# Kernel tuning notes

Hardware: AMD Instinct MI355X
Metric: run time of the kernel (lower is better)

## Reference

```python
import jax, jax.numpy as jnp
import numpy as np

B, S, H, R = 32, 1024, 1024, 53
EPS = 1e-12
ATT_EPS = 1e10


def setup_inputs() -> dict:
    key = jax.random.key(0)
    ks = jax.random.split(key, 20)
    sc = 0.02
    n = lambda k, shape: jax.random.normal(k, shape, jnp.float32) * sc
    return {
        "relation": jax.random.randint(ks[0], (B, 1), 0, R),
        "last_hidden_size": jax.random.normal(ks[1], (B, S, H), jnp.float32),
        "sub_head": jax.random.randint(ks[2], (B, 1), 0, S),
        "sub_tail": jax.random.randint(ks[3], (B, 1), 0, S),
        "attention_mask": jax.random.randint(ks[4], (B, S), 0, 2).astype(jnp.int32),
        # learned params
        "rel_emb": n(ks[5], (R, H)),
        "Wrf": n(ks[6], (H, H)), "brf": jnp.zeros((H,), jnp.float32),
        "cln_w": jnp.ones((H,), jnp.float32), "cln_b": jnp.zeros((H,), jnp.float32),
        "Wwd": n(ks[7], (H, 2 * H)), "Wbd": n(ks[8], (H, 2 * H)),
        "Wq": n(ks[9], (H, H)), "bq": jnp.zeros((H,), jnp.float32),
        "Wk": n(ks[10], (H, H)), "bk": jnp.zeros((H,), jnp.float32),
        "Wv": n(ks[11], (H, H)), "bv": jnp.zeros((H,), jnp.float32),
        "Wo": n(ks[12], (1, H)), "bo": jnp.zeros((1,), jnp.float32),
    }


def reference(relation, last_hidden_size, sub_head, sub_tail, attention_mask,
              rel_emb, Wrf, brf, cln_w, cln_b, Wwd, Wbd,
              Wq, bq, Wk, bk, Wv, bv, Wo, bo):
    x = last_hidden_size  # [B,S,H]; dropout is identity at inference
    # relation feature: embedding -> linear -> ReLU6
    rel = jnp.clip(jnp.einsum('boh,gh->bog', rel_emb[relation], Wrf) + brf, 0.0, 6.0)  # [B,1,H]
    # gather subject head/tail token features
    bidx = jnp.arange(x.shape[0])[:, None]
    sub = (x[bidx, sub_head] + x[bidx, sub_tail]) * 0.5  # [B,1,H]
    cond = jnp.concatenate([rel, sub], axis=-1)  # [B,1,2H]
    # conditional layer norm: per-example weight/bias generated from cond
    w = jnp.einsum('boc,gc->bog', cond, Wwd) + cln_w  # [B,1,H]
    b = jnp.einsum('boc,gc->bog', cond, Wbd) + cln_b  # [B,1,H]
    mean = jnp.mean(x, axis=-1, keepdims=True)
    c = x - mean
    var = jnp.mean(c * c, axis=-1, keepdims=True)
    normed = c / jnp.sqrt(var + EPS) * w + b  # [B,S,H]
    # ReLU-activated QKV attention with additive mask bias and residual
    q = jax.nn.relu(jnp.einsum('bsh,gh->bsg', normed, Wq) + bq)
    k = jax.nn.relu(jnp.einsum('bsh,gh->bsg', normed, Wk) + bk)
    v = jax.nn.relu(jnp.einsum('bsh,gh->bsg', normed, Wv) + bv)
    e = jnp.einsum('bsh,bth->bst', q, k)  # [B,S,S]
    m = attention_mask.astype(e.dtype)[:, None, :]  # [B,1,S]
    e = e - ATT_EPS * (1.0 - m)
    a = jax.nn.softmax(e, axis=-1)
    hidden = jnp.einsum('bst,bth->bsh', a, v) + normed  # [B,S,H]
    pred_obj_head = (jnp.einsum('bsh,gh->bsg', hidden, Wo) + bo)[..., 0]  # [B,S]
    return (pred_obj_head, hidden)
```

## Files before the change

### kernel.cpp

```cpp
#include <hip/hip_runtime.h>
#include <hip/hip_bf16.h>
#include <hip/hip_fp16.h>

#define NB 32
#define NS 1024
#define NH 1024

typedef short s16x4 __attribute__((ext_vector_type(4)));
typedef short s16x8 __attribute__((ext_vector_type(8)));
typedef float f32x4 __attribute__((ext_vector_type(4)));

typedef __attribute__((address_space(3))) void lds_void;
typedef const __attribute__((address_space(1))) void gmem_void;

__device__ __forceinline__ short f2bf(float f) {
  __hip_bfloat16 h = __float2bfloat16(f);
  return *reinterpret_cast<short*>(&h);
}
__device__ __forceinline__ float bf2f(short s) {
  union { unsigned u; float f; } cv;
  cv.u = ((unsigned)(unsigned short)s) << 16;
  return cv.f;
}
__device__ __forceinline__ short f2h(float f) {
  __half h = __float2half_rn(f);
  return *reinterpret_cast<short*>(&h);
}
__device__ __forceinline__ float h2f(short s) {
  __half h = *reinterpret_cast<__half*>(&s);
  return __half2float(h);
}

__device__ __forceinline__ float wave_reduce_sum(float v) {
#pragma unroll
  for (int o = 32; o; o >>= 1) v += __shfl_xor(v, o);
  return v;
}
__device__ __forceinline__ float wave_reduce_max(float v) {
#pragma unroll
  for (int o = 32; o; o >>= 1) v = fmaxf(v, __shfl_xor(v, o));
  return v;
}
__device__ __forceinline__ float block_reduce_sum(float v, float* red) {
  v = wave_reduce_sum(v);
  __syncthreads();
  if ((threadIdx.x & 63) == 0) red[threadIdx.x >> 6] = v;
  __syncthreads();
  return red[0] + red[1] + red[2] + red[3];
}
__device__ __forceinline__ float block_reduce_max(float v, float* red) {
  v = wave_reduce_max(v);
  __syncthreads();
  if ((threadIdx.x & 63) == 0) red[threadIdx.x >> 6] = v;
  __syncthreads();
  return fmaxf(fmaxf(red[0], red[1]), fmaxf(red[2], red[3]));
}


#define BAR1 do { __builtin_amdgcn_s_barrier();                              \
                  asm volatile("s_waitcnt lgkmcnt(0)" ::: "memory");         \
                  __builtin_amdgcn_sched_barrier(0); } while (0)
#define BAR2 do { __builtin_amdgcn_s_barrier();                              \
                  asm volatile("" ::: "memory"); } while (0)
#define VW   asm volatile("s_waitcnt vmcnt(4)" ::: "memory")
#define VW2  asm volatile("s_waitcnt vmcnt(2)" ::: "memory")
#define VW0  asm volatile("s_waitcnt vmcnt(0)" ::: "memory")

#define GEMM_PRE()                                                           \
  const int tid  = threadIdx.x;                                              \
  const int lane = tid & 63;                                                 \
  const int w    = tid >> 6;                                                 \
  const int wm   = w >> 2, wn = w & 3;                                       \
  const int fr   = lane & 15, fq = lane >> 4;                                \
  const long tA  = (long)(tid >> 3) * 1024 +                                 \
                   (((tid & 7) ^ ((tid >> 3) & 7)) << 3);                    \
  const int kc0  = (fq * 8) ^ ((fr & 7) * 8);                                \
  const int kc1  = (fq * 8 + 32) ^ ((fr & 7) * 8);                           \
  const int rdA  = wm * 8192 + fr * 64;                                      \
  const int rdB  = 16384 + (wn >> 1) * 8192 + (wn & 1) * 4096 + fr * 64;     \
  const int wsl  = w * 512;                                                  \
  f32x4 acc[8][4];                                                           \
  s16x8 aF[2][4][2], bF[2][2][2];                                            \
  _Pragma("unroll") for (int i_ = 0; i_ < 8; ++i_)                           \
    _Pragma("unroll") for (int j_ = 0; j_ < 4; ++j_)                         \
      acc[i_][j_] = (f32x4){0.f, 0.f, 0.f, 0.f};

#define STAGE(d, isB, h, kt)                                                 \
  do {                                                                       \
    const short* _g = ((isB) ? gB + (n0 + (h) * 128) * 1024                  \
                             : gA + (m0 + (h) * 128) * 1024) +               \
                      (long)(kt) * 64 + tA;                                  \
    short* _l = lds + (d) * 32768 + (isB) * 16384 + (h) * 8192 + wsl;        \
    __builtin_amdgcn_global_load_lds((gmem_void*)_g, (lds_void*)_l,          \
                                     16, 0, 0);                              \
    __builtin_amdgcn_global_load_lds((gmem_void*)(_g + 65536),               \
                                     (lds_void*)(_l + 4096), 16, 0, 0);      \
  } while (0)

#define RD_A(d, mq)                                                          \
  _Pragma("unroll") for (int mi = 0; mi < 4; ++mi) {                         \
    aF[mq][mi][0] = *(const s16x8*)(lds + (d) * 32768 + rdA + (mq) * 4096 +  \
                                    mi * 1024 + kc0);                        \
    aF[mq][mi][1] = *(const s16x8*)(lds + (d) * 32768 + rdA + (mq) * 4096 +  \
                                    mi * 1024 + kc1);                        \
  }
#define RD_B(d, nq)                                                          \
  _Pragma("unroll") for (int ni = 0; ni < 2; ++ni) {                         \
    bF[nq][ni][0] = *(const s16x8*)(lds + (d) * 32768 + rdB + (nq) * 2048 +  \
                                    ni * 1024 + kc0);                        \
    bF[nq][ni][1] = *(const s16x8*)(lds + (d) * 32768 + rdB + (nq) * 2048 +  \
                                    ni * 1024 + kc1);                        \
  }
#define MMA(mq, nq)                                                          \
  do {                                                                       \
    __builtin_amdgcn_s_setprio(1);                                           \
    _Pragma("unroll") for (int kk = 0; kk < 2; ++kk)                         \
      _Pragma("unroll") for (int mi = 0; mi < 4; ++mi)                       \
        _Pragma("unroll") for (int ni = 0; ni < 2; ++ni)                     \
          acc[(mq) * 4 + mi][(nq) * 2 + ni] =                                \
              __builtin_amdgcn_mfma_f32_16x16x32_bf16(                       \
                  aF[mq][mi][kk], bF[nq][ni][kk],                            \
                  acc[(mq) * 4 + mi][(nq) * 2 + ni], 0, 0, 0);               \
    __builtin_amdgcn_s_setprio(0);                                           \
  } while (0)

#define GEMM_MAIN()                                                          \
  GEMM_PRE();                                                                \
  STAGE(0, 1, 0, 0); STAGE(0, 1, 1, 0); STAGE(0, 0, 0, 0); STAGE(0, 0, 1, 0);\
  STAGE(1, 1, 0, 1); STAGE(1, 1, 1, 1);                                      \
  VW; BAR2;                                                                  \
  RD_A(0, 0);                                                                \
  for (int it = 0; it < 7; ++it) {                                           \
    const int t1 = 2 * it + 1, t2 = 2 * it + 2, t3 = 2 * it + 3;             \
    RD_B(0, 0); STAGE(1, 0, 0, t1); BAR1; MMA(0, 0); BAR2;                   \
    RD_B(0, 1); STAGE(1, 0, 1, t1); BAR1; MMA(0, 1); BAR2;                   \
    RD_A(0, 1); STAGE(0, 1, 0, t2); BAR1; MMA(1, 1); BAR2;                   \
    VW2;        STAGE(0, 1, 1, t2); BAR1; RD_A(1, 0); MMA(1, 0); BAR2;       \
    RD_B(1, 0); STAGE(0, 0, 0, t2); BAR1; MMA(0, 0); BAR2;                   \
    RD_B(1, 1); STAGE(0, 0, 1, t2); BAR1; MMA(0, 1); BAR2;                   \
    RD_A(1, 1); STAGE(1, 1, 0, t3); BAR1; MMA(1, 1); BAR2;                   \
    VW2;        STAGE(1, 1, 1, t3); BAR1; RD_A(0, 0); MMA(1, 0); BAR2;       \
  }                                                                          \
     \
  RD_B(0, 0); STAGE(1, 0, 0, 15); BAR1; MMA(0, 0); BAR2;                     \
  RD_B(0, 1); STAGE(1, 0, 1, 15); BAR1; MMA(0, 1); BAR2;                     \
  RD_A(0, 1);                     BAR1; MMA(1, 1); BAR2;                     \
  VW0;                            BAR1; RD_A(1, 0); MMA(1, 0); BAR2;         \
  RD_B(1, 0);                     BAR1; MMA(0, 0); BAR2;                     \
  RD_B(1, 1);                     BAR1; MMA(0, 1); BAR2;                     \
  RD_A(1, 1);                     BAR1; MMA(1, 1); BAR2;                     \
  VW0;                            BAR1; MMA(1, 0); BAR2;


__global__ __launch_bounds__(256) void prep_kernel(const int* __restrict__ relation,
    const float* __restrict__ x, const int* __restrict__ sub_head,
    const int* __restrict__ sub_tail, const float* __restrict__ rel_emb,
    const float* __restrict__ Wrf, const float* __restrict__ brf,
    float* __restrict__ cond,
    const float* __restrict__ Wq, const float* __restrict__ Wk,
    const float* __restrict__ Wv, short* __restrict__ wout) {
  const int blk = blockIdx.x;
  const int tid = threadIdx.x;
  if (blk >= 1056) {
    long i = ((long)(blk - 1056) * 256 + tid) * 4;
    int seg = (int)(i >> 20);
    long off = i & 1048575;
    const float* src = seg == 0 ? Wq : (seg == 1 ? Wk : Wv);
    f32x4 v = *(const f32x4*)(src + off);
    s16x4 o = { f2bf(v[0]), f2bf(v[1]), f2bf(v[2]), f2bf(v[3]) };
    *(s16x4*)(wout + i) = o;
    return;
  }
  if (blk >= 1024) {
    const int b = blk - 1024;
    const int sh = sub_head[b], st = sub_tail[b];
    for (int h = tid * 4; h < NH; h += 1024) {
      f32x4 a = *(const f32x4*)(x + ((long)b * NS + sh) * NH + h);
      f32x4 c = *(const f32x4*)(x + ((long)b * NS + st) * NH + h);
      f32x4 o = { 0.5f * (a[0] + c[0]), 0.5f * (a[1] + c[1]),
                  0.5f * (a[2] + c[2]), 0.5f * (a[3] + c[3]) };
      *(f32x4*)(cond + b * 2 * NH + NH + h) = o;
    }
    return;
  }
  const int g = blk;
  __shared__ float wr[NH];
  for (int h = tid * 4; h < NH; h += 1024)
    *(f32x4*)(wr + h) = *(const f32x4*)(Wrf + (long)g * NH + h);
  __syncthreads();
  const int lane = tid & 63, wid = tid >> 6;
  const float bg = brf[g];
  for (int b = wid; b < NB; b += 4) {
    const int rid = relation[b];
    const float* re = rel_emb + (long)rid * NH;
    float s = 0.f;
#pragma unroll
    for (int h = lane * 4; h < NH; h += 256) {
      f32x4 rv = *(const f32x4*)(re + h);
      f32x4 wv = *(const f32x4*)(wr + h);
      s += rv[0] * wv[0] + rv[1] * wv[1] + rv[2] * wv[2] + rv[3] * wv[3];
    }
    s = wave_reduce_sum(s);
    if (lane == 0) cond[b * 2 * NH + g] = fminf(fmaxf(s + bg, 0.f), 6.f);
  }
}

__global__ __launch_bounds__(256) void wb_kernel(const float* __restrict__ cond,
    const float* __restrict__ Wwd, const float* __restrict__ Wbd,
    const float* __restrict__ cln_w, const float* __restrict__ cln_b,
    float* __restrict__ wln, float* __restrict__ bln) {
  const int g = blockIdx.x;
  const int tid = threadIdx.x;
  __shared__ float wrow[2 * NH];
  __shared__ float brow[2 * NH];
  for (int i = tid * 4; i < 2 * NH; i += 1024) {
    *(f32x4*)(wrow + i) = *(const f32x4*)(Wwd + (long)g * 2 * NH + i);
    *(f32x4*)(brow + i) = *(const f32x4*)(Wbd + (long)g * 2 * NH + i);
  }
  __syncthreads();
  const int lane = tid & 63, wid = tid >> 6;
  const float cw = cln_w[g], cb = cln_b[g];
  for (int b = wid; b < NB; b += 4) {
    float sw = 0.f, sb = 0.f;
#pragma unroll
    for (int c = lane * 4; c < 2 * NH; c += 256) {
      f32x4 cv = *(const f32x4*)(cond + b * 2 * NH + c);
      f32x4 wv = *(const f32x4*)(wrow + c);
      f32x4 bv = *(const f32x4*)(brow + c);
      sw += cv[0] * wv[0] + cv[1] * wv[1] + cv[2] * wv[2] + cv[3] * wv[3];
      sb += cv[0] * bv[0] + cv[1] * bv[1] + cv[2] * bv[2] + cv[3] * bv[3];
    }
    sw = wave_reduce_sum(sw);
    sb = wave_reduce_sum(sb);
    if (lane == 0) {
      wln[b * NH + g] = sw + cw;
      bln[b * NH + g] = sb + cb;
    }
  }
}

__global__ __launch_bounds__(256) void ln_kernel(const float* __restrict__ x,
    const float* __restrict__ wln, const float* __restrict__ bln, short* __restrict__ normed) {
  const long row = blockIdx.x;
  const int tid = threadIdx.x;
  const long b = row >> 10;
  __shared__ float red[4];
  f32x4 v = *(const f32x4*)(x + row * NH + tid * 4);
  float mean = block_reduce_sum(v[0] + v[1] + v[2] + v[3], red) * (1.f / NH);
  float c0 = v[0] - mean, c1 = v[1] - mean, c2 = v[2] - mean, c3 = v[3] - mean;
  float var = block_reduce_sum(c0 * c0 + c1 * c1 + c2 * c2 + c3 * c3, red) * (1.f / NH);
  float rstd = rsqrtf(var + 1e-12f);
  f32x4 wv = *(const f32x4*)(wln + b * NH + tid * 4);
  f32x4 bv = *(const f32x4*)(bln + b * NH + tid * 4);
  s16x4 o = { f2bf(c0 * rstd * wv[0] + bv[0]), f2bf(c1 * rstd * wv[1] + bv[1]),
              f2bf(c2 * rstd * wv[2] + bv[2]), f2bf(c3 * rstd * wv[3] + bv[3]) };
  *(s16x4*)(normed + row * NH + tid * 4) = o;
}

__global__ __launch_bounds__(512, 2) void qkv_kernel(const short* __restrict__ A,
    const short* __restrict__ Wqkv,
    const float* __restrict__ bq, const float* __restrict__ bk, const float* __restrict__ bv,
    short* __restrict__ q, short* __restrict__ k, short* __restrict__ vT) {
  __shared__ short lds[67584];
  const int flat = blockIdx.y * 12 + blockIdx.x;
  const int gid  = (flat & 7) * 192 + (flat >> 3);
  const int mt = gid / 12, nt = gid % 12;
  const short* gA = A;
  const short* gB = Wqkv;
  const long n0 = (long)nt * 256;
  const long m0 = (long)mt * 256;
  GEMM_MAIN();
  const int z = nt >> 2;
  const long hc0 = (long)(nt & 3) * 256;
  const float* bias = z == 0 ? bq : (z == 1 ? bk : bv);
  if (z < 2) {
    short* dst = z == 0 ? q : k;
#pragma unroll
    for (int nI = 0; nI < 4; ++nI) {
      const long col = hc0 + wn * 64 + nI * 16 + fr;
      const float bcol = bias[col];
#pragma unroll
      for (int mI = 0; mI < 8; ++mI)
#pragma unroll
        for (int r = 0; r < 4; ++r) {
          const long row = m0 + wm * 128 + mI * 16 + fq * 4 + r;
          dst[row * NH + col] = f2bf(fmaxf(acc[mI][nI][r] + bcol, 0.f));
        }
    }
  } else {
    __syncthreads();
#pragma unroll
    for (int nI = 0; nI < 4; ++nI) {
      const int hl = wn * 64 + nI * 16 + fr;
      const float bcol = bias[hc0 + hl];
#pragma unroll
      for (int mI = 0; mI < 8; ++mI) {
        const int tl = wm * 128 + mI * 16 + fq * 4;
        s16x4 pk = { f2bf(fmaxf(acc[mI][nI][0] + bcol, 0.f)),
                     f2bf(fmaxf(acc[mI][nI][1] + bcol, 0.f)),
                     f2bf(fmaxf(acc[mI][nI][2] + bcol, 0.f)),
                     f2bf(fmaxf(acc[mI][nI][3] + bcol, 0.f)) };
        *(s16x4*)(lds + hl * 264 + tl) = pk;
      }
    }
    __syncthreads();
    const int h = tid >> 1, half = tid & 1;
    const long bb = m0 >> 10;
    short* dst = vT + ((bb * NH) + hc0 + h) * NS + (m0 & 1023) + half * 128;
    const short* src = lds + h * 264 + half * 128;
#pragma unroll
    for (int j = 0; j < 16; ++j)
      *(s16x8*)(dst + j * 8) = *(const s16x8*)(src + j * 8);
  }
}

__global__ __launch_bounds__(512, 2) void escore_kernel(const short* __restrict__ q,
    const short* __restrict__ k, const int* __restrict__ amask, short* __restrict__ e) {
  __shared__ short lds[65536];
  const int flat = blockIdx.z * 16 + blockIdx.y * 4 + blockIdx.x;
  const int gid  = (flat & 7) * 64 + (flat >> 3);
  const int b = gid >> 4, mt = (gid >> 2) & 3, nt = gid & 3;
  const short* gA = q + (long)b * NS * NH;
  const short* gB = k + (long)b * NS * NH;
  const long m0 = (long)mt * 256;
  const long n0 = (long)nt * 256;
  GEMM_MAIN();
  short* eb = e + (long)b * NS * NS;
#pragma unroll
  for (int mI = 0; mI < 8; ++mI)
#pragma unroll
    for (int nI = 0; nI < 4; ++nI) {
      const long col = n0 + wn * 64 + nI * 16 + fr;
      const float mb = -1e10f * (1.f - (float)amask[b * NS + col]) - 40.f;
#pragma unroll
      for (int r = 0; r < 4; ++r) {
        const long row = m0 + wm * 128 + mI * 16 + fq * 4 + r;
        eb[row * NS + col] = f2h(fmaxf(acc[mI][nI][r] + mb, -60000.f));
      }
    }
}

__global__ __launch_bounds__(256) void softmax_kernel(const short* __restrict__ e,
    short* __restrict__ a, float* __restrict__ inv_sum) {
  const long row = blockIdx.x;
  const int tid = threadIdx.x;
  __shared__ float red[4];
  s16x4 ev = *(const s16x4*)(e + row * NS + tid * 4);
  float v0 = h2f(ev[0]), v1 = h2f(ev[1]), v2 = h2f(ev[2]), v3 = h2f(ev[3]);
  float m = block_reduce_max(fmaxf(fmaxf(v0, v1), fmaxf(v2, v3)), red);
  float p0 = expf(v0 - m), p1 = expf(v1 - m);
  float p2 = expf(v2 - m), p3 = expf(v3 - m);
  float s = block_reduce_sum(p0 + p1 + p2 + p3, red);
  s16x4 o = { f2bf(p0), f2bf(p1), f2bf(p2), f2bf(p3) };
  *(s16x4*)(a + row * NS + tid * 4) = o;
  if (tid == 0) inv_sum[row] = 1.f / s;
}

__global__ __launch_bounds__(512, 2) void av_kernel(const short* __restrict__ a,
    const short* __restrict__ vT, const float* __restrict__ inv_sum,
    const short* __restrict__ normed, const float* __restrict__ Wo,
    float* __restrict__ hid, float* __restrict__ pred_part) {
  __shared__ short lds[65536];
  const int flat = blockIdx.z * 16 + blockIdx.y * 4 + blockIdx.x;
  const int gid  = (flat & 7) * 64 + (flat >> 3);
  const int b = gid >> 4, mt = (gid >> 2) & 3, nt = gid & 3;
  const short* gA = a + (long)b * NS * NS;
  const short* gB = vT + (long)b * NH * NS;
  const long m0 = (long)mt * 256;
  const long n0 = (long)nt * 256;
  GEMM_MAIN();
  float pp[8][4];
#pragma unroll
  for (int mI = 0; mI < 8; ++mI)
#pragma unroll
    for (int r = 0; r < 4; ++r) pp[mI][r] = 0.f;
#pragma unroll
  for (int nI = 0; nI < 4; ++nI) {
    const long col = n0 + wn * 64 + nI * 16 + fr;
    const float wo = Wo[col];
#pragma unroll
    for (int mI = 0; mI < 8; ++mI)
#pragma unroll
      for (int r = 0; r < 4; ++r) {
        const long row = m0 + wm * 128 + mI * 16 + fq * 4 + r;
        const long gi = ((long)b * NS + row) * NH + col;
        float hv = acc[mI][nI][r] * inv_sum[b * NS + row] + bf2f(normed[gi]);
        hid[gi] = hv;
        pp[mI][r] += hv * wo;
      }
  }
#pragma unroll
  for (int mI = 0; mI < 8; ++mI)
#pragma unroll
    for (int r = 0; r < 4; ++r) {
      float v = pp[mI][r];
      v += __shfl_xor(v, 1);
      v += __shfl_xor(v, 2);
      v += __shfl_xor(v, 4);
      v += __shfl_xor(v, 8);
      if (fr == 0)
        pred_part[((long)nt * 4 + wn) * (NB * NS) + (long)b * NS + m0 +
                  wm * 128 + mI * 16 + fq * 4 + r] = v;
    }
}

__global__ __launch_bounds__(256) void pred_finish_kernel(const float* __restrict__ pp,
    const float* __restrict__ bo, float* __restrict__ pred) {
  const int i = (blockIdx.x * 256 + threadIdx.x) * 4;
  const float bz = bo[0];
  f32x4 o = { bz, bz, bz, bz };
#pragma unroll
  for (int j = 0; j < 16; ++j) {
    f32x4 a = *(const f32x4*)(pp + (long)j * (NB * NS) + i);
    o[0] += a[0]; o[1] += a[1]; o[2] += a[2]; o[3] += a[3];
  }
  *(f32x4*)(pred + i) = o;
}

extern "C" void kernel_launch(void* const* d_in, const int* in_sizes, int n_in,
                              void* d_out, int out_size, void* d_ws, size_t ws_size,
                              hipStream_t stream) {
  (void)in_sizes; (void)n_in; (void)out_size; (void)ws_size;
  const int*   relation = (const int*)d_in[0];
  const float* x        = (const float*)d_in[1];
  const int*   sub_head = (const int*)d_in[2];
  const int*   sub_tail = (const int*)d_in[3];
  const int*   amask    = (const int*)d_in[4];
  const float* rel_emb  = (const float*)d_in[5];
  const float* Wrf      = (const float*)d_in[6];
  const float* brf      = (const float*)d_in[7];
  const float* cln_w    = (const float*)d_in[8];
  const float* cln_b    = (const float*)d_in[9];
  const float* Wwd      = (const float*)d_in[10];
  const float* Wbd      = (const float*)d_in[11];
  const float* Wq       = (const float*)d_in[12];
  const float* bq       = (const float*)d_in[13];
  const float* Wk       = (const float*)d_in[14];
  const float* bk       = (const float*)d_in[15];
  const float* Wv       = (const float*)d_in[16];
  const float* bv       = (const float*)d_in[17];
  const float* Wo       = (const float*)d_in[18];
  const float* bo       = (const float*)d_in[19];

  char* ws = (char*)d_ws;
  short* wqkv_bf = (short*)ws;
  float* cond    = (float*)(ws + 6291456);
  float* wln     = cond + 32 * 2048;
  float* bln     = wln + 32 * 1024;
  float* inv_sum = bln + 32 * 1024;
  short* normed  = (short*)(inv_sum + 32768);
  short* qb      = normed + 33554432;
  short* kb      = qb + 33554432;
  short* vT      = kb + 33554432;
  short* e       = vT + 33554432;
  float* pred_part = (float*)(e + 33554432);

  float* pred = (float*)d_out;
  float* hid  = pred + 32768;

  prep_kernel<<<4128, 256, 0, stream>>>(relation, x, sub_head, sub_tail,
                                        rel_emb, Wrf, brf, cond,
                                        Wq, Wk, Wv, wqkv_bf);
  wb_kernel<<<NH, 256, 0, stream>>>(cond, Wwd, Wbd, cln_w, cln_b, wln, bln);
  ln_kernel<<<NB * NS, 256, 0, stream>>>(x, wln, bln, normed);
  qkv_kernel<<<dim3(12, 128), 512, 0, stream>>>(normed, wqkv_bf,
                                                bq, bk, bv, qb, kb, vT);
  escore_kernel<<<dim3(4, 4, 32), 512, 0, stream>>>(qb, kb, amask, e);
  softmax_kernel<<<NB * NS, 256, 0, stream>>>(e, qb, inv_sum);
  av_kernel<<<dim3(4, 4, 32), 512, 0, stream>>>(qb, vT, inv_sum, normed, Wo,
                                                hid, pred_part);
  pred_finish_kernel<<<32, 256, 0, stream>>>(pred_part, bo, pred);
}
```

Before: 499.1 us.

## Halve GEMM K-tile to 32 to double occupancy in attention GEMMs

Adds a GEMM variant that stages 32-wide K slices instead of 64, halving shared memory per block to 64KB. The escore and av kernels switch to it and declare 4 blocks per CU instead of 2, aiming to hide latency through more resident waves. In exchange there are twice as many pipeline steps and barriers per tile, and the tighter launch bound caps registers per thread, which could cause spills given the 128-float accumulator.

```diff
diff --git a/kernel.cpp b/kernel.cpp
--- a/kernel.cpp
+++ b/kernel.cpp
@@ -55,7 +55,6 @@
   __syncthreads();
   return fmaxf(fmaxf(red[0], red[1]), fmaxf(red[2], red[3]));
 }
-
 
 #define BAR1 do { __builtin_amdgcn_s_barrier();                              \
                   asm volatile("s_waitcnt lgkmcnt(0)" ::: "memory");         \
@@ -64,6 +63,7 @@
                   asm volatile("" ::: "memory"); } while (0)
 #define VW   asm volatile("s_waitcnt vmcnt(4)" ::: "memory")
 #define VW2  asm volatile("s_waitcnt vmcnt(2)" ::: "memory")
+#define VW1  asm volatile("s_waitcnt vmcnt(1)" ::: "memory")
 #define VW0  asm volatile("s_waitcnt vmcnt(0)" ::: "memory")
 
 #define GEMM_PRE()                                                           \
@@ -141,7 +141,6 @@
     RD_A(1, 1); STAGE(1, 1, 0, t3); BAR1; MMA(1, 1); BAR2;                   \
     VW2;        STAGE(1, 1, 1, t3); BAR1; RD_A(0, 0); MMA(1, 0); BAR2;       \
   }                                                                          \
-     \
   RD_B(0, 0); STAGE(1, 0, 0, 15); BAR1; MMA(0, 0); BAR2;                     \
   RD_B(0, 1); STAGE(1, 0, 1, 15); BAR1; MMA(0, 1); BAR2;                     \
   RD_A(0, 1);                     BAR1; MMA(1, 1); BAR2;                     \
@@ -150,6 +149,82 @@
   RD_B(1, 1);                     BAR1; MMA(0, 1); BAR2;                     \
   RD_A(1, 1);                     BAR1; MMA(1, 1); BAR2;                     \
   VW0;                            BAR1; MMA(1, 0); BAR2;
+
+#define GEMM32_PRE()                                                         \
+  const int tid  = threadIdx.x;                                              \
+  const int lane = tid & 63;                                                 \
+  const int w    = tid >> 6;                                                 \
+  const int wm   = w >> 2, wn = w & 3;                                       \
+  const int fr   = lane & 15, fq = lane >> 4;                                \
+  const long tA32 = (long)(tid >> 2) * 1024 +                                \
+                    (((tid & 3) ^ ((tid >> 3) & 3)) << 3);                   \
+  const int kc32 = (fq ^ ((fr >> 1) & 3)) << 3;                              \
+  const int rdA32 = wm * 4096 + fr * 32 + kc32;                              \
+  const int rdB32 = 8192 + (wn >> 1) * 4096 + (wn & 1) * 2048 +              \
+                    fr * 32 + kc32;                                          \
+  const int wsl32 = w * 512;                                                 \
+  f32x4 acc[8][4];                                                           \
+  s16x8 aF2[2][4], bF2[2][2];                                                \
+  _Pragma("unroll") for (int i_ = 0; i_ < 8; ++i_)                           \
+    _Pragma("unroll") for (int j_ = 0; j_ < 4; ++j_)                         \
+      acc[i_][j_] = (f32x4){0.f, 0.f, 0.f, 0.f};
+
+#define STAGE32(d, isB, h, kt)                                               \
+  do {                                                                       \
+    const short* _g = ((isB) ? gB + (n0 + (h) * 128) * 1024                  \
+                             : gA + (m0 + (h) * 128) * 1024) +               \
+                      (long)(kt) * 32 + tA32;                                \
+    short* _l = lds + (d) * 16384 + (isB) * 8192 + (h) * 4096 + wsl32;       \
+    __builtin_amdgcn_global_load_lds((gmem_void*)_g, (lds_void*)_l,          \
+                                     16, 0, 0);                              \
+  } while (0)
+
+#define RD_A32(d, mq)                                                        \
+  _Pragma("unroll") for (int mi = 0; mi < 4; ++mi)                           \
+    aF2[mq][mi] = *(const s16x8*)(lds + (d) * 16384 + rdA32 +                \
+                                  (mq) * 2048 + mi * 512);
+#define RD_B32(d, nq)                                                        \
+  _Pragma("unroll") for (int ni = 0; ni < 2; ++ni)                           \
+    bF2[nq][ni] = *(const s16x8*)(lds + (d) * 16384 + rdB32 +                \
+                                  (nq) * 1024 + ni * 512);
+#define MMA32(mq, nq)                                                        \
+  do {                                                                       \
+    __builtin_amdgcn_s_setprio(1);                                           \
+    _Pragma("unroll") for (int mi = 0; mi < 4; ++mi)                         \
+      _Pragma("unroll") for (int ni = 0; ni < 2; ++ni)                       \
+        acc[(mq) * 4 + mi][(nq) * 2 + ni] =                                  \
+            __builtin_amdgcn_mfma_f32_16x16x32_bf16(                         \
+                aF2[mq][mi], bF2[nq][ni],                                    \
+                acc[(mq) * 4 + mi][(nq) * 2 + ni], 0, 0, 0);                 \
+    __builtin_amdgcn_s_setprio(0);                                           \
+  } while (0)
+
+#define GEMM32_MAIN()                                                        \
+  GEMM32_PRE();                                                              \
+  STAGE32(0, 1, 0, 0); STAGE32(0, 1, 1, 0);                                  \
+  STAGE32(0, 0, 0, 0); STAGE32(0, 0, 1, 0);                                  \
+  STAGE32(1, 1, 0, 1); STAGE32(1, 1, 1, 1);                                  \
+  VW2; BAR2;                                                                 \
+  RD_A32(0, 0);                                                              \
+  for (int it = 0; it < 15; ++it) {                                          \
+    const int t1 = 2 * it + 1, t2 = 2 * it + 2, t3 = 2 * it + 3;             \
+    RD_B32(0, 0); STAGE32(1, 0, 0, t1); BAR1; MMA32(0, 0); BAR2;             \
+    RD_B32(0, 1); STAGE32(1, 0, 1, t1); BAR1; MMA32(0, 1); BAR2;             \
+    RD_A32(0, 1); STAGE32(0, 1, 0, t2); BAR1; MMA32(1, 1); BAR2;             \
+    VW1;          STAGE32(0, 1, 1, t2); BAR1; RD_A32(1, 0); MMA32(1, 0); BAR2;\
+    RD_B32(1, 0); STAGE32(0, 0, 0, t2); BAR1; MMA32(0, 0); BAR2;             \
+    RD_B32(1, 1); STAGE32(0, 0, 1, t2); BAR1; MMA32(0, 1); BAR2;             \
+    RD_A32(1, 1); STAGE32(1, 1, 0, t3); BAR1; MMA32(1, 1); BAR2;             \
+    VW1;          STAGE32(1, 1, 1, t3); BAR1; RD_A32(0, 0); MMA32(1, 0); BAR2;\
+  }                                                                          \
+  RD_B32(0, 0); STAGE32(1, 0, 0, 31); BAR1; MMA32(0, 0); BAR2;               \
+  RD_B32(0, 1); STAGE32(1, 0, 1, 31); BAR1; MMA32(0, 1); BAR2;               \
+  RD_A32(0, 1);                       BAR1; MMA32(1, 1); BAR2;               \
+  VW0;                                BAR1; RD_A32(1, 0); MMA32(1, 0); BAR2; \
+  RD_B32(1, 0);                       BAR1; MMA32(0, 0); BAR2;               \
+  RD_B32(1, 1);                       BAR1; MMA32(0, 1); BAR2;               \
+  RD_A32(1, 1);                       BAR1; MMA32(1, 1); BAR2;               \
+  VW0;                                BAR1; MMA32(1, 0); BAR2;
 
 
 __global__ __launch_bounds__(256) void prep_kernel(const int* __restrict__ relation,
@@ -314,9 +389,9 @@
   }
 }
 
-__global__ __launch_bounds__(512, 2) void escore_kernel(const short* __restrict__ q,
+__global__ __launch_bounds__(512, 4) void escore_kernel(const short* __restrict__ q,
     const short* __restrict__ k, const int* __restrict__ amask, short* __restrict__ e) {
-  __shared__ short lds[65536];
+  __shared__ short lds[32768];
   const int flat = blockIdx.z * 16 + blockIdx.y * 4 + blockIdx.x;
   const int gid  = (flat & 7) * 64 + (flat >> 3);
   const int b = gid >> 4, mt = (gid >> 2) & 3, nt = gid & 3;
@@ -324,7 +399,7 @@
   const short* gB = k + (long)b * NS * NH;
   const long m0 = (long)mt * 256;
   const long n0 = (long)nt * 256;
-  GEMM_MAIN();
+  GEMM32_MAIN();
   short* eb = e + (long)b * NS * NS;
 #pragma unroll
   for (int mI = 0; mI < 8; ++mI)
@@ -356,11 +431,11 @@
   if (tid == 0) inv_sum[row] = 1.f / s;
 }
 
-__global__ __launch_bounds__(512, 2) void av_kernel(const short* __restrict__ a,
+__global__ __launch_bounds__(512, 4) void av_kernel(const short* __restrict__ a,
     const short* __restrict__ vT, const float* __restrict__ inv_sum,
     const short* __restrict__ normed, const float* __restrict__ Wo,
     float* __restrict__ hid, float* __restrict__ pred_part) {
-  __shared__ short lds[65536];
+  __shared__ short lds[32768];
   const int flat = blockIdx.z * 16 + blockIdx.y * 4 + blockIdx.x;
   const int gid  = (flat & 7) * 64 + (flat >> 3);
   const int b = gid >> 4, mt = (gid >> 2) & 3, nt = gid & 3;
@@ -368,7 +443,7 @@
   const short* gB = vT + (long)b * NH * NS;
   const long m0 = (long)mt * 256;
   const long n0 = (long)nt * 256;
-  GEMM_MAIN();
+  GEMM32_MAIN();
   float pp[8][4];
 #pragma unroll
   for (int mI = 0; mI < 8; ++mI)
```

Result: slower. 1.980 ms (+296.7%).
